# Kernel tuning notes

Measured on AMD Instinct MI355X. Metric: run time of the kernel, lower is better.

## Reference

```python
import jax, jax.numpy as jnp
import numpy as np

B, T, D, H, C = 128, 256, 256, 1024, 10


def setup_inputs() -> dict:
    key = jax.random.key(0)
    ks = jax.random.split(key, 11)
    std = 1.0 / T  # matches nn.init.normal_(std=1/seq_length)
    inp = {
        'x':   jax.random.normal(ks[0], (B, T, D), dtype=jnp.float32),
        'Wfx': jax.random.normal(ks[1], (D, H), dtype=jnp.float32) * std,
        'Wix': jax.random.normal(ks[2], (D, H), dtype=jnp.float32) * std,
        'Wgx': jax.random.normal(ks[3], (D, H), dtype=jnp.float32) * std,
        'Wox': jax.random.normal(ks[4], (D, H), dtype=jnp.float32) * std,
        'Wfh': jax.random.normal(ks[5], (H, H), dtype=jnp.float32) * std,
        'Wih': jax.random.normal(ks[6], (H, H), dtype=jnp.float32) * std,
        'Wgh': jax.random.normal(ks[7], (H, H), dtype=jnp.float32) * std,
        'Woh': jax.random.normal(ks[8], (H, H), dtype=jnp.float32) * std,
        'bf':  jnp.zeros((H,), jnp.float32),
        'bi':  jnp.zeros((H,), jnp.float32),
        'bg':  jnp.zeros((H,), jnp.float32),
        'bo':  jnp.zeros((H,), jnp.float32),
        'Wph': jax.random.normal(ks[9], (H, C), dtype=jnp.float32) * std,
        'bp':  jnp.zeros((C,), jnp.float32),
    }
    return inp


def reference(x, Wfx, Wix, Wgx, Wox, Wfh, Wih, Wgh, Woh, bf, bi, bg, bo, Wph, bp):
    b, t, d = x.shape
    h = Wfh.shape[0]
    # Fuse the 4 input-side and 4 hidden-side matmuls into two big GEMMs per step
    Wx = jnp.concatenate([Wfx, Wix, Wgx, Wox], axis=1)  # [D, 4H]
    Wh = jnp.concatenate([Wfh, Wih, Wgh, Woh], axis=1)  # [H, 4H]
    bb = jnp.concatenate([bf, bi, bg, bo])              # [4H]

    # Precompute all input projections in one batched GEMM: [T, B, 4H]
    xg = jnp.einsum('btd,dk->tbk', x, Wx) + bb

    def step(carry, xgt):
        hs, cs = carry
        gates = xgt + hs @ Wh  # [B, 4H]
        f = jax.nn.sigmoid(gates[:, 0 * h:1 * h])
        i = jax.nn.sigmoid(gates[:, 1 * h:2 * h])
        g = jnp.tanh(gates[:, 2 * h:3 * h])
        o = jax.nn.sigmoid(gates[:, 3 * h:4 * h])
        cs = g * i + cs * f
        hs = jnp.tanh(cs) * o
        return (hs, cs), None

    h0 = jnp.zeros((b, h), x.dtype)
    c0 = jnp.zeros((b, h), x.dtype)
    (hT, _), _ = jax.lax.scan(step, (h0, c0), xg)
    return hT @ Wph + bp
```

## Files before the change

### kernel.cpp

```cpp
#include <hip/hip_runtime.h>
#include <math.h>


#define BB 128
#define TT 256
#define DD 256
#define HH 1024
#define NKT 40
#define KHT 20
#define PFA 4
#define PFB 5

typedef __bf16 bf16x8 __attribute__((ext_vector_type(8)));
typedef float  f32x4  __attribute__((ext_vector_type(4)));
typedef unsigned short u16;
typedef u16 u16x8 __attribute__((ext_vector_type(8)));

__device__ __forceinline__ u16 f2bf(float f){
  unsigned u = __builtin_bit_cast(unsigned, f);
  u += 0x7fffu + ((u >> 16) & 1u);
  return (u16)(u >> 16);
}
__device__ __forceinline__ float bf2f(u16 b){
  unsigned u = ((unsigned)b) << 16;
  return __builtin_bit_cast(float, u);
}
__device__ __forceinline__ float sigm(float x){
  return 1.f / (1.f + __expf(-x));
}
__device__ __forceinline__ float tanh_fast(float x){
  return 2.f / (1.f + __expf(-2.f * x)) - 1.f;
}
__device__ __forceinline__ int swzb(int slot){
  return slot ^ ((slot >> 6) & 7) ^ (((slot >> 4) & 3) << 1);
}

__global__ void prep_wpack(const float* __restrict__ Wfx, const float* __restrict__ Wix,
                           const float* __restrict__ Wgx, const float* __restrict__ Wox,
                           const float* __restrict__ Wfh, const float* __restrict__ Wih,
                           const float* __restrict__ Wgh, const float* __restrict__ Woh,
                           u16* __restrict__ Wpack){
  int id = blockIdx.x * 256 + threadIdx.x;
  int lane = id & 63;
  int kt = (id >> 6) % NKT;
  int ct = id / (64 * NKT);
  int col = ct * 16 + (lane & 15);
  int g = col >> 10, n = col & 1023;
  int kbase = kt * 32 + (lane >> 4) * 8;
  const float* Wx = (g==0) ? Wfx : (g==1) ? Wix : (g==2) ? Wgx : Wox;
  const float* Wh = (g==0) ? Wfh : (g==1) ? Wih : (g==2) ? Wgh : Woh;
  u16x8 v;
  #pragma unroll
  for (int j = 0; j < 8; ++j){
    int k = kbase + j;
    float f = (k < DD) ? Wx[k * HH + n] : Wh[(k - DD) * HH + n];
    v[j] = f2bf(f);
  }
  *(u16x8*)(Wpack + (size_t)id * 8) = v;
}

__global__ void prep_xT(const float* __restrict__ x, u16* __restrict__ xT){
  int id = blockIdx.x * 256 + threadIdx.x;
  int t = id >> 12;
  int b = (id >> 5) & 127;
  int d0 = (id & 31) * 8;
  const float* src = x + ((size_t)b * TT + t) * DD + d0;
  u16x8 v;
  #pragma unroll
  for (int j = 0; j < 8; ++j) v[j] = f2bf(src[j]);
  *(u16x8*)(xT + (size_t)id * 8) = v;
}

__global__ __launch_bounds__(512, 4) void lstm_step(
    const u16* __restrict__ xTt,
    const u16* __restrict__ Wpack,
    const u16* __restrict__ hin,
    u16* __restrict__ hout,
    float* __restrict__ cbuf,
    const float* __restrict__ bfv, const float* __restrict__ biv,
    const float* __restrict__ bgv, const float* __restrict__ bov){
  __shared__ u16x8 As4[NKT * 64];
  __shared__ float pLds0[16][68];
  __shared__ float pLds1[16][68];
  const int tid = threadIdx.x;
  const int bx = blockIdx.x;
  const int n0 = bx * 16;
  const int m0 = blockIdx.y * 16;

  const int crow = tid >> 4, cnn = tid & 15;
  const int gi = (m0 + (crow & 15)) * HH + n0 + cnn;
  float cprev = 0.f;
  if (tid < 256) cprev = cbuf[gi];

  const int w = tid >> 6, lane = tid & 63, cr = lane & 15, q4 = lane >> 4;
  const int g  = w & 3;
  const int kh = w >> 2;
  const int ktBeg = kh * KHT;

  const u16x8* wq = (const u16x8*)Wpack + (size_t)(g * 64 + bx) * NKT * 64 + lane;
  u16x8 aP[PFA], bP[PFB];
  #pragma unroll
  for (int i = 0; i < PFB; ++i) bP[i] = wq[(size_t)(ktBeg + i) * 64];

  #pragma unroll
  for (int it = 0; it < 5; ++it){
    int ch = tid + it * 512;
    int m = ch / 160;
    int k0 = (ch - m * 160) * 8;
    const u16* src = (k0 < DD) ? (xTt + (m0 + m) * DD + k0)
                               : (hin + (m0 + m) * HH + (k0 - DD));
    u16x8 val = *(const u16x8*)src;
    int kt = k0 >> 5, q = (k0 >> 3) & 3;
    As4[swzb(kt * 64 + 16 * q + m)] = val;
  }
  __syncthreads();

  #pragma unroll
  for (int i = 0; i < PFA; ++i) aP[i] = As4[swzb((ktBeg + i) * 64 + lane)];

  f32x4 acc = {0.f, 0.f, 0.f, 0.f};
  #pragma unroll
  for (int kt = 0; kt < KHT; ++kt){
    u16x8 ac = aP[kt % PFA], b = bP[kt % PFB];
    if (kt + PFA < KHT)
      aP[kt % PFA] = As4[swzb((ktBeg + kt + PFA) * 64 + lane)];
    if (kt + PFB < KHT)
      bP[kt % PFB] = wq[(size_t)(ktBeg + kt + PFB) * 64];
    acc = __builtin_amdgcn_mfma_f32_16x16x32_bf16(__builtin_bit_cast(bf16x8, ac),
            __builtin_bit_cast(bf16x8, b), acc, 0, 0, 0);
  }

  if (!kh){
    const float* bptr = (g==0) ? bfv : (g==1) ? biv : (g==2) ? bgv : bov;
    const float bias = bptr[n0 + cr];
    #pragma unroll
    for (int r = 0; r < 4; ++r)
      pLds0[q4 * 4 + r][g * 16 + cr] = acc[r] + bias;
  } else {
    #pragma unroll
    for (int r = 0; r < 4; ++r)
      pLds1[q4 * 4 + r][g * 16 + cr] = acc[r];
  }
  __syncthreads();

  if (tid < 256){
    float fp = pLds0[crow][cnn]      + pLds1[crow][cnn];
    float ip = pLds0[crow][16 + cnn] + pLds1[crow][16 + cnn];
    float gp = pLds0[crow][32 + cnn] + pLds1[crow][32 + cnn];
    float op = pLds0[crow][48 + cnn] + pLds1[crow][48 + cnn];
    float fs = sigm(fp);
    float is = sigm(ip);
    float gs = tanh_fast(gp);
    float os = sigm(op);
    float cn = gs * is + cprev * fs;
    cbuf[gi] = cn;
    hout[gi] = f2bf(tanh_fast(cn) * os);
  }
}

__global__ void final_proj(const u16* __restrict__ h, const float* __restrict__ Wph,
                           const float* __restrict__ bp, float* __restrict__ out){
  __shared__ float red[10][256];
  int b = blockIdx.x, tid = threadIdx.x;
  float p[10];
  #pragma unroll
  for (int c = 0; c < 10; ++c) p[c] = 0.f;
  for (int k = tid; k < HH; k += 256){
    float hv = bf2f(h[b * HH + k]);
    const float* wr = Wph + (size_t)k * 10;
    #pragma unroll
    for (int c = 0; c < 10; ++c) p[c] += hv * wr[c];
  }
  #pragma unroll
  for (int c = 0; c < 10; ++c) red[c][tid] = p[c];
  __syncthreads();
  for (int s = 128; s > 0; s >>= 1){
    if (tid < s){
      #pragma unroll
      for (int c = 0; c < 10; ++c) red[c][tid] += red[c][tid + s];
    }
    __syncthreads();
  }
  if (tid < 10) out[b * 10 + tid] = red[tid][0] + bp[tid];
}

extern "C" void kernel_launch(void* const* d_in, const int* in_sizes, int n_in,
                              void* d_out, int out_size, void* d_ws, size_t ws_size,
                              hipStream_t stream){
  (void)in_sizes; (void)n_in; (void)out_size; (void)ws_size;
  const float* x   = (const float*)d_in[0];
  const float* Wfx = (const float*)d_in[1];
  const float* Wix = (const float*)d_in[2];
  const float* Wgx = (const float*)d_in[3];
  const float* Wox = (const float*)d_in[4];
  const float* Wfh = (const float*)d_in[5];
  const float* Wih = (const float*)d_in[6];
  const float* Wgh = (const float*)d_in[7];
  const float* Woh = (const float*)d_in[8];
  const float* bfv = (const float*)d_in[9];
  const float* biv = (const float*)d_in[10];
  const float* bgv = (const float*)d_in[11];
  const float* bov = (const float*)d_in[12];
  const float* Wph = (const float*)d_in[13];
  const float* bp  = (const float*)d_in[14];

  char* ws = (char*)d_ws;
  u16*  Wpack = (u16*)ws;
  u16*  xT    = (u16*)(ws + 10485760);
  u16*  h0    = (u16*)(ws + 27262976);
  u16*  h1    = (u16*)(ws + 27525120);
  float* cb   = (float*)(ws + 27787264);

  prep_wpack<<<2560, 256, 0, stream>>>(Wfx, Wix, Wgx, Wox, Wfh, Wih, Wgh, Woh, Wpack);
  prep_xT<<<4096, 256, 0, stream>>>(x, xT);
  hipMemsetAsync(h0, 0, 262144, stream);
  hipMemsetAsync(cb, 0, 524288, stream);

  for (int t = 0; t < TT; ++t){
    const u16* hin  = (t & 1) ? h1 : h0;
    u16*       hout = (t & 1) ? h0 : h1;
    lstm_step<<<dim3(64, 8), 512, 0, stream>>>(xT + (size_t)t * BB * DD, Wpack,
                                               hin, hout, cb, bfv, biv, bgv, bov);
  }
  final_proj<<<128, 256, 0, stream>>>(h0, Wph, bp, (float*)d_out);
}
```

Before: 1.880 ms.

## Double batch rows per block and split K four ways with 1024 threads

```diff
diff --git a/kernel.cpp b/kernel.cpp
--- a/kernel.cpp
+++ b/kernel.cpp
@@ -7,7 +7,7 @@
 #define DD 256
 #define HH 1024
 #define NKT 40
-#define KHT 20
+#define KQT 10
 #define PFA 4
 #define PFB 5
 
@@ -71,7 +71,7 @@
   *(u16x8*)(xT + (size_t)id * 8) = v;
 }
 
-__global__ __launch_bounds__(512, 4) void lstm_step(
+__global__ __launch_bounds__(1024, 1) void lstm_step(
     const u16* __restrict__ xTt,
     const u16* __restrict__ Wpack,
     const u16* __restrict__ hin,
@@ -79,75 +79,95 @@
     float* __restrict__ cbuf,
     const float* __restrict__ bfv, const float* __restrict__ biv,
     const float* __restrict__ bgv, const float* __restrict__ bov){
-  __shared__ u16x8 As4[NKT * 64];
-  __shared__ float pLds0[16][68];
-  __shared__ float pLds1[16][68];
+  __shared__ u16x8 AsLo[NKT * 64];
+  __shared__ u16x8 AsHi[NKT * 64];
+  __shared__ float pLds[4][32][68];
   const int tid = threadIdx.x;
   const int bx = blockIdx.x;
   const int n0 = bx * 16;
-  const int m0 = blockIdx.y * 16;
+  const int m0 = blockIdx.y * 32;
 
   const int crow = tid >> 4, cnn = tid & 15;
-  const int gi = (m0 + (crow & 15)) * HH + n0 + cnn;
+  const int gi = (m0 + (crow & 31)) * HH + n0 + cnn;
   float cprev = 0.f;
-  if (tid < 256) cprev = cbuf[gi];
+  if (tid < 512) cprev = cbuf[gi];
 
   const int w = tid >> 6, lane = tid & 63, cr = lane & 15, q4 = lane >> 4;
   const int g  = w & 3;
-  const int kh = w >> 2;
-  const int ktBeg = kh * KHT;
+  const int kq = w >> 2;
+  const int ktBeg = kq * KQT;
 
   const u16x8* wq = (const u16x8*)Wpack + (size_t)(g * 64 + bx) * NKT * 64 + lane;
-  u16x8 aP[PFA], bP[PFB];
+  u16x8 bP[PFB];
   #pragma unroll
   for (int i = 0; i < PFB; ++i) bP[i] = wq[(size_t)(ktBeg + i) * 64];
 
   #pragma unroll
   for (int it = 0; it < 5; ++it){
-    int ch = tid + it * 512;
-    int m = ch / 160;
-    int k0 = (ch - m * 160) * 8;
-    const u16* src = (k0 < DD) ? (xTt + (m0 + m) * DD + k0)
-                               : (hin + (m0 + m) * HH + (k0 - DD));
+    int ch = tid + it * 1024;
+    int hi = (ch >= 2560) ? 1 : 0;
+    int ch2 = ch - hi * 2560;
+    int m = ch2 / 160;
+    int k0 = (ch2 - m * 160) * 8;
+    int row = m0 + hi * 16 + m;
+    const u16* src = (k0 < DD) ? (xTt + row * DD + k0)
+                               : (hin + row * HH + (k0 - DD));
     u16x8 val = *(const u16x8*)src;
     int kt = k0 >> 5, q = (k0 >> 3) & 3;
-    As4[swzb(kt * 64 + 16 * q + m)] = val;
+    int slot = swzb(kt * 64 + 16 * q + m);
+    if (hi) AsHi[slot] = val; else AsLo[slot] = val;
   }
   __syncthreads();
 
-  #pragma unroll
-  for (int i = 0; i < PFA; ++i) aP[i] = As4[swzb((ktBeg + i) * 64 + lane)];
-
-  f32x4 acc = {0.f, 0.f, 0.f, 0.f};
-  #pragma unroll
-  for (int kt = 0; kt < KHT; ++kt){
-    u16x8 ac = aP[kt % PFA], b = bP[kt % PFB];
-    if (kt + PFA < KHT)
-      aP[kt % PFA] = As4[swzb((ktBeg + kt + PFA) * 64 + lane)];
-    if (kt + PFB < KHT)
+  u16x8 aLoP[PFA], aHiP[PFA];
+  #pragma unroll
+  for (int i = 0; i < PFA; ++i){
+    aLoP[i] = AsLo[swzb((ktBeg + i) * 64 + lane)];
+    aHiP[i] = AsHi[swzb((ktBeg + i) * 64 + lane)];
+  }
+
+  f32x4 accLo = {0.f, 0.f, 0.f, 0.f}, accHi = {0.f, 0.f, 0.f, 0.f};
+  #pragma unroll
+  for (int kt = 0; kt < KQT; ++kt){
+    u16x8 alo = aLoP[kt % PFA], ahi = aHiP[kt % PFA], b = bP[kt % PFB];
+    if (kt + PFA < KQT){
+      aLoP[kt % PFA] = AsLo[swzb((ktBeg + kt + PFA) * 64 + lane)];
+      aHiP[kt % PFA] = AsHi[swzb((ktBeg + kt + PFA) * 64 + lane)];
+    }
+    if (kt + PFB < KQT)
       bP[kt % PFB] = wq[(size_t)(ktBeg + kt + PFB) * 64];
-    acc = __builtin_amdgcn_mfma_f32_16x16x32_bf16(__builtin_bit_cast(bf16x8, ac),
-            __builtin_bit_cast(bf16x8, b), acc, 0, 0, 0);
-  }
-
-  if (!kh){
+    accLo = __builtin_amdgcn_mfma_f32_16x16x32_bf16(__builtin_bit_cast(bf16x8, alo),
+              __builtin_bit_cast(bf16x8, b), accLo, 0, 0, 0);
+    accHi = __builtin_amdgcn_mfma_f32_16x16x32_bf16(__builtin_bit_cast(bf16x8, ahi),
+              __builtin_bit_cast(bf16x8, b), accHi, 0, 0, 0);
+  }
+
+  if (kq == 0){
     const float* bptr = (g==0) ? bfv : (g==1) ? biv : (g==2) ? bgv : bov;
     const float bias = bptr[n0 + cr];
     #pragma unroll
-    for (int r = 0; r < 4; ++r)
-      pLds0[q4 * 4 + r][g * 16 + cr] = acc[r] + bias;
+    for (int r = 0; r < 4; ++r){
+      pLds[0][q4 * 4 + r][g * 16 + cr]      = accLo[r] + bias;
+      pLds[0][16 + q4 * 4 + r][g * 16 + cr] = accHi[r] + bias;
+    }
   } else {
     #pragma unroll
-    for (int r = 0; r < 4; ++r)
-      pLds1[q4 * 4 + r][g * 16 + cr] = acc[r];
+    for (int r = 0; r < 4; ++r){
+      pLds[kq][q4 * 4 + r][g * 16 + cr]      = accLo[r];
+      pLds[kq][16 + q4 * 4 + r][g * 16 + cr] = accHi[r];
+    }
   }
   __syncthreads();
 
-  if (tid < 256){
-    float fp = pLds0[crow][cnn]      + pLds1[crow][cnn];
-    float ip = pLds0[crow][16 + cnn] + pLds1[crow][16 + cnn];
-    float gp = pLds0[crow][32 + cnn] + pLds1[crow][32 + cnn];
-    float op = pLds0[crow][48 + cnn] + pLds1[crow][48 + cnn];
+  if (tid < 512){
+    float fp = pLds[0][crow][cnn]      + pLds[1][crow][cnn]
+             + pLds[2][crow][cnn]      + pLds[3][crow][cnn];
+    float ip = pLds[0][crow][16 + cnn] + pLds[1][crow][16 + cnn]
+             + pLds[2][crow][16 + cnn] + pLds[3][crow][16 + cnn];
+    float gp = pLds[0][crow][32 + cnn] + pLds[1][crow][32 + cnn]
+             + pLds[2][crow][32 + cnn] + pLds[3][crow][32 + cnn];
+    float op = pLds[0][crow][48 + cnn] + pLds[1][crow][48 + cnn]
+             + pLds[2][crow][48 + cnn] + pLds[3][crow][48 + cnn];
     float fs = sigm(fp);
     float is = sigm(ip);
     float gs = tanh_fast(gp);
@@ -219,8 +239,8 @@
   for (int t = 0; t < TT; ++t){
     const u16* hin  = (t & 1) ? h1 : h0;
     u16*       hout = (t & 1) ? h0 : h1;
-    lstm_step<<<dim3(64, 8), 512, 0, stream>>>(xT + (size_t)t * BB * DD, Wpack,
-                                               hin, hout, cb, bfv, biv, bgv, bov);
+    lstm_step<<<dim3(64, 4), 1024, 0, stream>>>(xT + (size_t)t * BB * DD, Wpack,
+                                                hin, hout, cb, bfv, biv, bgv, bov);
   }
   final_proj<<<128, 256, 0, stream>>>(h0, Wph, bp, (float*)d_out);
 }
```

Measured after the change: 1.716 ms. 8.7% less time.
